# Kernel tuning notes

Measured on AMD Instinct MI355X. Metric: run time of the kernel, lower is better.

## Reference

```python
import jax, jax.numpy as jnp
import numpy as np

HIDDEN = 2048
IN = 2
OUT = 2
T = 1024


def setup_inputs() -> dict:
    key = jax.random.key(0)
    ks = jax.random.split(key, 8)
    s_ih = 1.0 / np.sqrt(HIDDEN)
    return {
        "features": jax.random.normal(ks[0], (1, HIDDEN), dtype=jnp.float32),
        "point_cloud": jax.random.normal(ks[1], (1, T, IN), dtype=jnp.float32),
        "W_ih": jax.random.uniform(ks[2], (4 * HIDDEN, IN), jnp.float32, -s_ih, s_ih),
        "W_hh": jax.random.uniform(ks[3], (4 * HIDDEN, HIDDEN), jnp.float32, -s_ih, s_ih),
        "b_ih": jax.random.uniform(ks[4], (4 * HIDDEN,), jnp.float32, -s_ih, s_ih),
        "b_hh": jax.random.uniform(ks[5], (4 * HIDDEN,), jnp.float32, -s_ih, s_ih),
        "W_fc": jax.random.uniform(ks[6], (OUT, HIDDEN), jnp.float32, -s_ih, s_ih),
        "b_fc": jax.random.uniform(ks[7], (OUT,), jnp.float32, -s_ih, s_ih),
        "max_seq_len": T,
    }


def reference(features, point_cloud, W_ih, W_hh, b_ih, b_hh, W_fc, b_fc, max_seq_len):
    # Training branch of DecoderRNN.forward: teacher-forced LSTMCell decode.
    H = features.shape[1]
    c0 = jnp.zeros_like(features)  # [B, H]

    def step(carry, x_t):
        h, c = carry
        gates = x_t @ W_ih.T + b_ih + h @ W_hh.T + b_hh  # [B, 4H]
        i, f, g, o = jnp.split(gates, 4, axis=-1)  # PyTorch LSTMCell gate order
        c_new = jax.nn.sigmoid(f) * c + jax.nn.sigmoid(i) * jnp.tanh(g)
        h_new = jax.nn.sigmoid(o) * jnp.tanh(c_new)
        out = h_new @ W_fc.T + b_fc  # [B, OUT]
        return (h_new, c_new), out

    xs = jnp.swapaxes(point_cloud, 0, 1)  # [T, B, IN]
    _, outs = jax.lax.scan(step, (features, c0), xs)  # outs: [T, B, OUT]
    # original returns outputs[:, 1:, :] which drops the initial zeros row
    return jnp.swapaxes(outs, 0, 1)  # [B, T, OUT]
```

## Files before the change

### kernel.cpp

```cpp
#include <hip/hip_runtime.h>
#include <math.h>
#include <stdint.h>

#define HIDDEN 2048
#define TSTEPS 1024
#define NWG 256
#define TPB 512
#define UPW 8
#define CPT 16
#define FLAG_STRIDE 32

__device__ __forceinline__ float sigmoidf_(float x) { return 1.0f / (1.0f + __expf(-x)); }

__global__ __launch_bounds__(TPB, 2)
void lstm_hist(const float* __restrict__ features,
               const float* __restrict__ pc,
               const float* __restrict__ W_ih,
               const float* __restrict__ W_hh,
               const float* __restrict__ b_ih,
               const float* __restrict__ b_hh,
               const float* __restrict__ W_fc,
               const float* __restrict__ b_fc,
               float* __restrict__ out,
               int*   __restrict__ flags,
               int*   __restrict__ go,
               float* __restrict__ hhist)
{
    const int b    = blockIdx.x;
    const int t    = threadIdx.x;
    const int lane = t & 63;
    const int wave = t >> 6;

    __builtin_amdgcn_fence(__ATOMIC_ACQUIRE, "agent");

    const int g    = t & 3;
    const int cc   = t >> 2;
    const int col0 = cc * CPT;
    const bool watcher = (b == NWG - 1) && (wave == 0);

    __shared__ float pc_sh[2 * TSTEPS];
    __shared__ float red[8 * 32];
    __shared__ float outred[16];

    {
        const float4* p4 = reinterpret_cast<const float4*>(pc);
        reinterpret_cast<float4*>(pc_sh)[t] = p4[t];
    }

    float w[UPW][CPT];
    {
        const int baserow = g * HIDDEN + b * UPW;
        #pragma unroll
        for (int ji = 0; ji < UPW; ++ji) {
            const float4* src = reinterpret_cast<const float4*>(
                W_hh + (size_t)(baserow + ji) * HIDDEN + col0);
            float4 a0 = src[0], a1 = src[1], a2 = src[2], a3 = src[3];
            w[ji][0]  = a0.x; w[ji][1]  = a0.y; w[ji][2]  = a0.z; w[ji][3]  = a0.w;
            w[ji][4]  = a1.x; w[ji][5]  = a1.y; w[ji][6]  = a1.z; w[ji][7]  = a1.w;
            w[ji][8]  = a2.x; w[ji][9]  = a2.y; w[ji][10] = a2.z; w[ji][11] = a2.w;
            w[ji][12] = a3.x; w[ji][13] = a3.y; w[ji][14] = a3.z; w[ji][15] = a3.w;
        }
    }

    float bias_r = 0.0f, wi0_r = 0.0f, wi1_r = 0.0f, creg = 0.0f;
    if (wave == 0) {
        const int l   = lane & 31;
        const int row = (l >> 3) * HIDDEN + b * UPW + (l & 7);
        bias_r = b_ih[row] + b_hh[row];
        wi0_r  = W_ih[row * 2 + 0];
        wi1_r  = W_ih[row * 2 + 1];
    }
    __syncthreads();

    for (int s = 0; s < TSTEPS; ++s) {
        const int rot = (s >= 1) && (b == ((s - 1) & 255));
        const float* hsrc = (s == 0) ? features : (hhist + (size_t)s * HIDDEN);

        float hr[CPT];
        #pragma unroll
        for (int k = 0; k < CPT; k += 4) {
            float4 hv = *reinterpret_cast<const float4*>(hsrc + col0 + k);
            hr[k] = hv.x; hr[k + 1] = hv.y; hr[k + 2] = hv.z; hr[k + 3] = hv.w;
        }

        float acc[UPW];
        #pragma unroll
        for (int ji = 0; ji < UPW; ++ji) acc[ji] = 0.0f;
        #pragma unroll
        for (int k = 0; k < CPT; ++k) {
            #pragma unroll
            for (int ji = 0; ji < UPW; ++ji) acc[ji] += w[ji][k] * hr[k];
        }
        #pragma unroll
        for (int m = 4; m < 64; m <<= 1) {
            #pragma unroll
            for (int ji = 0; ji < UPW; ++ji) acc[ji] += __shfl_xor(acc[ji], m);
        }
        if (lane < 4) {
            #pragma unroll
            for (int ji = 0; ji < UPW; ++ji) red[wave * 32 + lane * 8 + ji] = acc[ji];
        }

        if (rot) {
            float po0 = 0.0f, po1 = 0.0f;
            #pragma unroll
            for (int k = 0; k < CPT; ++k) {
                po0 += hr[k] * W_fc[col0 + k];
                po1 += hr[k] * W_fc[HIDDEN + col0 + k];
            }
            #pragma unroll
            for (int m = 1; m < 64; m <<= 1) {
                po0 += __shfl_xor(po0, m);
                po1 += __shfl_xor(po1, m);
            }
            if (lane == 0) { outred[wave * 2 + 0] = po0; outred[wave * 2 + 1] = po1; }
        }
        __syncthreads();

        if (wave == 0) {
            const int l = lane & 31;
            float sum = 0.0f;
            #pragma unroll
            for (int ww = 0; ww < 8; ++ww) sum += red[ww * 32 + l];
            const float x0 = pc_sh[2 * s], x1 = pc_sh[2 * s + 1];
            const float gate = sum + bias_r + wi0_r * x0 + wi1_r * x1;
            const float iv = __shfl(gate, (lane & 7));
            const float fv = __shfl(gate, 8 + (lane & 7));
            const float gv = __shfl(gate, 16 + (lane & 7));
            const float ov = __shfl(gate, 24 + (lane & 7));
            const float cnew = sigmoidf_(fv) * creg + sigmoidf_(iv) * tanhf(gv);
            const float hnew = sigmoidf_(ov) * tanhf(cnew);
            creg = cnew;
            const uint32_t hb = __float_as_uint(hnew);

            const uint32_t lo = __shfl(hb, 2 * (lane & 3));
            const uint32_t hi = __shfl(hb, 2 * (lane & 3) + 1);
            if (lane < 4) {
                const uint64_t qv = (uint64_t)lo | ((uint64_t)hi << 32);
                uint64_t* dst = reinterpret_cast<uint64_t*>(
                    hhist + (size_t)(s + 1) * HIDDEN + b * UPW) + lane;
                __hip_atomic_store(dst, qv, __ATOMIC_RELAXED, __HIP_MEMORY_SCOPE_AGENT);
            }
            asm volatile("s_waitcnt vmcnt(0)" ::: "memory");
            if (lane == 0) {
                __hip_atomic_store(flags + (size_t)b * FLAG_STRIDE, s + 1,
                                   __ATOMIC_RELAXED, __HIP_MEMORY_SCOPE_AGENT);
            }
        }

        if (rot && t == 64) {
            float o0 = 0.0f, o1 = 0.0f;
            #pragma unroll
            for (int ww = 0; ww < 8; ++ww) { o0 += outred[ww * 2]; o1 += outred[ww * 2 + 1]; }
            out[(s - 1) * 2 + 0] = 0.25f * o0 + b_fc[0];
            out[(s - 1) * 2 + 1] = 0.25f * o1 + b_fc[1];
        }

        if (watcher) {
            const int l4 = lane * 4;
            const int* f0p = flags + (size_t)(l4 + 0) * FLAG_STRIDE;
            const int* f1p = flags + (size_t)(l4 + 1) * FLAG_STRIDE;
            const int* f2p = flags + (size_t)(l4 + 2) * FLAG_STRIDE;
            const int* f3p = flags + (size_t)(l4 + 3) * FLAG_STRIDE;
            for (;;) {
                const int f0 = __hip_atomic_load(f0p, __ATOMIC_RELAXED, __HIP_MEMORY_SCOPE_AGENT);
                const int f1 = __hip_atomic_load(f1p, __ATOMIC_RELAXED, __HIP_MEMORY_SCOPE_AGENT);
                const int f2 = __hip_atomic_load(f2p, __ATOMIC_RELAXED, __HIP_MEMORY_SCOPE_AGENT);
                const int f3 = __hip_atomic_load(f3p, __ATOMIC_RELAXED, __HIP_MEMORY_SCOPE_AGENT);
                const bool ok = (f0 >= s + 1) & (f1 >= s + 1) & (f2 >= s + 1) & (f3 >= s + 1);
                if (__all(ok)) break;
            }
            __hip_atomic_store(go + (size_t)lane * FLAG_STRIDE, s + 1,
                               __ATOMIC_RELAXED, __HIP_MEMORY_SCOPE_AGENT);
        }

        if (t == 0) {
            const int* gop = go + (size_t)(b >> 2) * FLAG_STRIDE;
            while (__hip_atomic_load(gop, __ATOMIC_RELAXED,
                                     __HIP_MEMORY_SCOPE_AGENT) < s + 1) {
                __builtin_amdgcn_s_sleep(1);
            }
        }
        __syncthreads();
    }

    if (b == ((TSTEPS - 1) & 255)) {
        const float* hsrc = hhist + (size_t)TSTEPS * HIDDEN;
        float po0 = 0.0f, po1 = 0.0f;
        #pragma unroll
        for (int k = 0; k < CPT; ++k) {
            const float hv = hsrc[col0 + k];
            po0 += hv * W_fc[col0 + k];
            po1 += hv * W_fc[HIDDEN + col0 + k];
        }
        #pragma unroll
        for (int m = 1; m < 64; m <<= 1) {
            po0 += __shfl_xor(po0, m);
            po1 += __shfl_xor(po1, m);
        }
        if (lane == 0) { outred[wave * 2 + 0] = po0; outred[wave * 2 + 1] = po1; }
        __syncthreads();
        if (t == 0) {
            float o0 = 0.0f, o1 = 0.0f;
            #pragma unroll
            for (int ww = 0; ww < 8; ++ww) { o0 += outred[ww * 2]; o1 += outred[ww * 2 + 1]; }
            out[(TSTEPS - 1) * 2 + 0] = 0.25f * o0 + b_fc[0];
            out[(TSTEPS - 1) * 2 + 1] = 0.25f * o1 + b_fc[1];
        }
    }
}

extern "C" void kernel_launch(void* const* d_in, const int* in_sizes, int n_in,
                              void* d_out, int out_size, void* d_ws, size_t ws_size,
                              hipStream_t stream) {
    const float* features = (const float*)d_in[0];
    const float* pc       = (const float*)d_in[1];
    const float* W_ih     = (const float*)d_in[2];
    const float* W_hh     = (const float*)d_in[3];
    const float* b_ih     = (const float*)d_in[4];
    const float* b_hh     = (const float*)d_in[5];
    const float* W_fc     = (const float*)d_in[6];
    const float* b_fc     = (const float*)d_in[7];
    float* out = (float*)d_out;

    const size_t flags_bytes = (size_t)NWG * FLAG_STRIDE * sizeof(int);
    const size_t go_bytes    = (size_t)64 * FLAG_STRIDE * sizeof(int);
    const size_t hh_off      = flags_bytes + go_bytes;

    int*   flags = (int*)d_ws;
    int*   go    = (int*)((char*)d_ws + flags_bytes);
    float* hhist = (float*)((char*)d_ws + hh_off);

    hipMemsetAsync(d_ws, 0, hh_off, stream);

    hipLaunchKernelGGL(lstm_hist, dim3(NWG), dim3(TPB), 0, stream,
                       features, pc, W_ih, W_hh, b_ih, b_hh, W_fc, b_fc,
                       out, flags, go, hhist);
}
```

Before: 3.595 ms.

## Pack tagged h values into per-block messages and have watcher republish hidden state

Each workgroup now writes its eight new hidden values as 16-bit halves packed together with a step tag into six 64-bit words, using parity double buffering. A dedicated watcher wave polls these tagged messages, which removes the separate flag store and its preceding waitcnt. The watcher then writes the values into the h-history buffer and releases the go flags. The spin wait also drops s_sleep. Hidden state is still stored as full fp32 bit patterns, split into two halves per value. The watcher now does more loads and stores, which lengthens its critical path and may cost more than the removed flag round trip.

```diff
diff --git a/kernel.cpp b/kernel.cpp
--- a/kernel.cpp
+++ b/kernel.cpp
@@ -8,7 +8,9 @@
 #define TPB 512
 #define UPW 8
 #define CPT 16
-#define FLAG_STRIDE 32
+#define LINE_QW 6
+#define LINE_STRIDE_QW 16
+#define GO_STRIDE 32
 
 __device__ __forceinline__ float sigmoidf_(float x) { return 1.0f / (1.0f + __expf(-x)); }
 
@@ -22,9 +24,9 @@
                const float* __restrict__ W_fc,
                const float* __restrict__ b_fc,
                float* __restrict__ out,
-               int*   __restrict__ flags,
-               int*   __restrict__ go,
-               float* __restrict__ hhist)
+               uint64_t* __restrict__ msg,
+               int*      __restrict__ go,
+               float*    __restrict__ hhist)
 {
     const int b    = blockIdx.x;
     const int t    = threadIdx.x;
@@ -36,7 +38,6 @@
     const int g    = t & 3;
     const int cc   = t >> 2;
     const int col0 = cc * CPT;
-    const bool watcher = (b == NWG - 1) && (wave == 0);
 
     __shared__ float pc_sh[2 * TSTEPS];
     __shared__ float red[8 * 32];
@@ -116,6 +117,8 @@
             if (lane == 0) { outred[wave * 2 + 0] = po0; outred[wave * 2 + 1] = po1; }
         }
         __syncthreads();
+
+        const int par = ((s + 1) & 1) * 8;
 
         if (wave == 0) {
             const int l = lane & 31;
@@ -133,19 +136,67 @@
             creg = cnew;
             const uint32_t hb = __float_as_uint(hnew);
 
-            const uint32_t lo = __shfl(hb, 2 * (lane & 3));
-            const uint32_t hi = __shfl(hb, 2 * (lane & 3) + 1);
-            if (lane < 4) {
-                const uint64_t qv = (uint64_t)lo | ((uint64_t)hi << 32);
-                uint64_t* dst = reinterpret_cast<uint64_t*>(
-                    hhist + (size_t)(s + 1) * HIDDEN + b * UPW) + lane;
-                __hip_atomic_store(dst, qv, __ATOMIC_RELAXED, __HIP_MEMORY_SCOPE_AGENT);
+            uint64_t v = ((uint64_t)(uint32_t)(s + 1)) << 48;
+            #pragma unroll
+            for (int i = 0; i < 3; ++i) {
+                const int m  = 3 * lane + i;
+                const int mc = (m < 16) ? m : 15;
+                const uint32_t bits = __shfl(hb, mc >> 1);
+                const uint32_t half = (mc & 1) ? (bits >> 16) : (bits & 0xFFFFu);
+                if (m < 16) v |= (uint64_t)half << (32 - 16 * i);
+            }
+            if (lane < LINE_QW) {
+                __hip_atomic_store(msg + (size_t)b * LINE_STRIDE_QW + par + lane,
+                                   v, __ATOMIC_RELAXED, __HIP_MEMORY_SCOPE_AGENT);
+            }
+        }
+
+        if (b == NWG - 1 && wave == 7) {
+            const int l4 = lane * 4;
+            const uint32_t tagexp = (uint32_t)(s + 1);
+            uint64_t q[4][LINE_QW];
+            for (;;) {
+                #pragma unroll
+                for (int i = 0; i < 4; ++i) {
+                    const uint64_t* lp = msg + (size_t)(l4 + i) * LINE_STRIDE_QW + par;
+                    #pragma unroll
+                    for (int j = 0; j < LINE_QW; ++j) {
+                        q[i][j] = __hip_atomic_load(lp + j, __ATOMIC_RELAXED,
+                                                    __HIP_MEMORY_SCOPE_AGENT);
+                    }
+                }
+                bool ok = true;
+                #pragma unroll
+                for (int i = 0; i < 4; ++i) {
+                    #pragma unroll
+                    for (int j = 0; j < LINE_QW; ++j) {
+                        ok &= ((uint32_t)(q[i][j] >> 48) == tagexp);
+                    }
+                }
+                if (ok) break;
+            }
+            uint64_t* hq = reinterpret_cast<uint64_t*>(hhist + (size_t)(s + 1) * HIDDEN);
+            #pragma unroll
+            for (int i = 0; i < 4; ++i) {
+                uint32_t H[18];
+                #pragma unroll
+                for (int j = 0; j < LINE_QW; ++j) {
+                    H[3 * j + 0] = (uint32_t)(q[i][j] >> 32) & 0xFFFFu;
+                    H[3 * j + 1] = (uint32_t)(q[i][j] >> 16) & 0xFFFFu;
+                    H[3 * j + 2] = (uint32_t)(q[i][j] >>  0) & 0xFFFFu;
+                }
+                #pragma unroll
+                for (int k = 0; k < 4; ++k) {
+                    const uint32_t f0 = H[4 * k + 0] | (H[4 * k + 1] << 16);
+                    const uint32_t f1 = H[4 * k + 2] | (H[4 * k + 3] << 16);
+                    __hip_atomic_store(hq + (size_t)(l4 + i) * 4 + k,
+                                       (uint64_t)f0 | ((uint64_t)f1 << 32),
+                                       __ATOMIC_RELAXED, __HIP_MEMORY_SCOPE_AGENT);
+                }
             }
             asm volatile("s_waitcnt vmcnt(0)" ::: "memory");
-            if (lane == 0) {
-                __hip_atomic_store(flags + (size_t)b * FLAG_STRIDE, s + 1,
-                                   __ATOMIC_RELAXED, __HIP_MEMORY_SCOPE_AGENT);
-            }
+            __hip_atomic_store(go + (size_t)lane * GO_STRIDE, s + 1,
+                               __ATOMIC_RELAXED, __HIP_MEMORY_SCOPE_AGENT);
         }
 
         if (rot && t == 64) {
@@ -156,30 +207,10 @@
             out[(s - 1) * 2 + 1] = 0.25f * o1 + b_fc[1];
         }
 
-        if (watcher) {
-            const int l4 = lane * 4;
-            const int* f0p = flags + (size_t)(l4 + 0) * FLAG_STRIDE;
-            const int* f1p = flags + (size_t)(l4 + 1) * FLAG_STRIDE;
-            const int* f2p = flags + (size_t)(l4 + 2) * FLAG_STRIDE;
-            const int* f3p = flags + (size_t)(l4 + 3) * FLAG_STRIDE;
-            for (;;) {
-                const int f0 = __hip_atomic_load(f0p, __ATOMIC_RELAXED, __HIP_MEMORY_SCOPE_AGENT);
-                const int f1 = __hip_atomic_load(f1p, __ATOMIC_RELAXED, __HIP_MEMORY_SCOPE_AGENT);
-                const int f2 = __hip_atomic_load(f2p, __ATOMIC_RELAXED, __HIP_MEMORY_SCOPE_AGENT);
-                const int f3 = __hip_atomic_load(f3p, __ATOMIC_RELAXED, __HIP_MEMORY_SCOPE_AGENT);
-                const bool ok = (f0 >= s + 1) & (f1 >= s + 1) & (f2 >= s + 1) & (f3 >= s + 1);
-                if (__all(ok)) break;
-            }
-            __hip_atomic_store(go + (size_t)lane * FLAG_STRIDE, s + 1,
-                               __ATOMIC_RELAXED, __HIP_MEMORY_SCOPE_AGENT);
-        }
-
-        if (t == 0) {
-            const int* gop = go + (size_t)(b >> 2) * FLAG_STRIDE;
+        if (t == 0 && b != NWG - 1) {
+            const int* gop = go + (size_t)(b >> 2) * GO_STRIDE;
             while (__hip_atomic_load(gop, __ATOMIC_RELAXED,
-                                     __HIP_MEMORY_SCOPE_AGENT) < s + 1) {
-                __builtin_amdgcn_s_sleep(1);
-            }
+                                     __HIP_MEMORY_SCOPE_AGENT) < s + 1) {}
         }
         __syncthreads();
     }
@@ -223,17 +254,17 @@
     const float* b_fc     = (const float*)d_in[7];
     float* out = (float*)d_out;
 
-    const size_t flags_bytes = (size_t)NWG * FLAG_STRIDE * sizeof(int);
-    const size_t go_bytes    = (size_t)64 * FLAG_STRIDE * sizeof(int);
-    const size_t hh_off      = flags_bytes + go_bytes;
-
-    int*   flags = (int*)d_ws;
-    int*   go    = (int*)((char*)d_ws + flags_bytes);
-    float* hhist = (float*)((char*)d_ws + hh_off);
+    const size_t msg_bytes = (size_t)NWG * LINE_STRIDE_QW * sizeof(uint64_t);
+    const size_t go_bytes  = (size_t)64 * GO_STRIDE * sizeof(int);
+    const size_t hh_off    = msg_bytes + go_bytes;
+
+    uint64_t* msg   = (uint64_t*)d_ws;
+    int*      go    = (int*)((char*)d_ws + msg_bytes);
+    float*    hhist = (float*)((char*)d_ws + hh_off);
 
     hipMemsetAsync(d_ws, 0, hh_off, stream);
 
     hipLaunchKernelGGL(lstm_hist, dim3(NWG), dim3(TPB), 0, stream,
                        features, pc, W_ih, W_hh, b_ih, b_hh, W_fc, b_fc,
-                       out, flags, go, hhist);
+                       out, msg, go, hhist);
 }
```

Measured after the change: 5.983 ms. +66.4%, slower.

## Replace per-step block barrier with per-thread spin on grid go flags

Applied to the files above, without the earlier changes.

The end-of-step __syncthreads and the single-thread sleep-poll on the go flag are removed. Every thread now spins directly on its group's go flag (or on an LDS flag in the watcher block) just before loading the next hidden state. The watcher moves to wave 7 of the last block and also publishes progress through LDS. This targets the latency of the grid-wide step handoff: the barrier and s_sleep wake-up delay. In exchange, all threads poll global memory, which adds memory traffic, and correctness now depends on the flag ordering rather than an explicit barrier for reuse of the shared reduction buffers.

```diff
diff --git a/kernel.cpp b/kernel.cpp
--- a/kernel.cpp
+++ b/kernel.cpp
@@ -9,38 +9,41 @@
 #define UPW 8
 #define CPT 16
 #define FLAG_STRIDE 32
+#define GO_STRIDE 32
 
 __device__ __forceinline__ float sigmoidf_(float x) { return 1.0f / (1.0f + __expf(-x)); }
 
 __global__ __launch_bounds__(TPB, 2)
-void lstm_hist(const float* __restrict__ features,
-               const float* __restrict__ pc,
-               const float* __restrict__ W_ih,
-               const float* __restrict__ W_hh,
-               const float* __restrict__ b_ih,
-               const float* __restrict__ b_hh,
-               const float* __restrict__ W_fc,
-               const float* __restrict__ b_fc,
-               float* __restrict__ out,
-               int*   __restrict__ flags,
-               int*   __restrict__ go,
-               float* __restrict__ hhist)
+void lstm_v10(const float* __restrict__ features,
+              const float* __restrict__ pc,
+              const float* __restrict__ W_ih,
+              const float* __restrict__ W_hh,
+              const float* __restrict__ b_ih,
+              const float* __restrict__ b_hh,
+              const float* __restrict__ W_fc,
+              const float* __restrict__ b_fc,
+              float* __restrict__ out,
+              int*   __restrict__ flags,
+              int*   __restrict__ go,
+              float* __restrict__ hhist)
 {
     const int b    = blockIdx.x;
     const int t    = threadIdx.x;
     const int lane = t & 63;
     const int wave = t >> 6;
-
-    __builtin_amdgcn_fence(__ATOMIC_ACQUIRE, "agent");
-
     const int g    = t & 3;
     const int cc   = t >> 2;
     const int col0 = cc * CPT;
-    const bool watcher = (b == NWG - 1) && (wave == 0);
+    const bool isw255 = (b == NWG - 1);
+
+    __builtin_amdgcn_fence(__ATOMIC_ACQUIRE, "agent");
 
     __shared__ float pc_sh[2 * TSTEPS];
     __shared__ float red[8 * 32];
     __shared__ float outred[16];
+    __shared__ int   ls_go;
+
+    if (t == 0) ls_go = 0;
 
     {
         const float4* p4 = reinterpret_cast<const float4*>(pc);
@@ -72,15 +75,32 @@
     }
     __syncthreads();
 
+    const int* gop = go + (size_t)(b >> 2) * GO_STRIDE;
+
     for (int s = 0; s < TSTEPS; ++s) {
         const int rot = (s >= 1) && (b == ((s - 1) & 255));
-        const float* hsrc = (s == 0) ? features : (hhist + (size_t)s * HIDDEN);
 
         float hr[CPT];
-        #pragma unroll
-        for (int k = 0; k < CPT; k += 4) {
-            float4 hv = *reinterpret_cast<const float4*>(hsrc + col0 + k);
-            hr[k] = hv.x; hr[k + 1] = hv.y; hr[k + 2] = hv.z; hr[k + 3] = hv.w;
+        if (s == 0) {
+            #pragma unroll
+            for (int k = 0; k < CPT; k += 4) {
+                float4 hv = *reinterpret_cast<const float4*>(features + col0 + k);
+                hr[k] = hv.x; hr[k + 1] = hv.y; hr[k + 2] = hv.z; hr[k + 3] = hv.w;
+            }
+        } else {
+            if (isw255) {
+                while (__hip_atomic_load(&ls_go, __ATOMIC_RELAXED,
+                                         __HIP_MEMORY_SCOPE_WORKGROUP) < s) {}
+            } else {
+                while (__hip_atomic_load(gop, __ATOMIC_RELAXED,
+                                         __HIP_MEMORY_SCOPE_AGENT) < s) {}
+            }
+            const float* hsrc = hhist + (size_t)s * HIDDEN;
+            #pragma unroll
+            for (int k = 0; k < CPT; k += 4) {
+                float4 hv = *reinterpret_cast<const float4*>(hsrc + col0 + k);
+                hr[k] = hv.x; hr[k + 1] = hv.y; hr[k + 2] = hv.z; hr[k + 3] = hv.w;
+            }
         }
 
         float acc[UPW];
@@ -148,15 +168,7 @@
             }
         }
 
-        if (rot && t == 64) {
-            float o0 = 0.0f, o1 = 0.0f;
-            #pragma unroll
-            for (int ww = 0; ww < 8; ++ww) { o0 += outred[ww * 2]; o1 += outred[ww * 2 + 1]; }
-            out[(s - 1) * 2 + 0] = 0.25f * o0 + b_fc[0];
-            out[(s - 1) * 2 + 1] = 0.25f * o1 + b_fc[1];
-        }
-
-        if (watcher) {
+        if (isw255 && wave == 7) {
             const int l4 = lane * 4;
             const int* f0p = flags + (size_t)(l4 + 0) * FLAG_STRIDE;
             const int* f1p = flags + (size_t)(l4 + 1) * FLAG_STRIDE;
@@ -170,21 +182,26 @@
                 const bool ok = (f0 >= s + 1) & (f1 >= s + 1) & (f2 >= s + 1) & (f3 >= s + 1);
                 if (__all(ok)) break;
             }
-            __hip_atomic_store(go + (size_t)lane * FLAG_STRIDE, s + 1,
+            __hip_atomic_store(go + (size_t)lane * GO_STRIDE, s + 1,
                                __ATOMIC_RELAXED, __HIP_MEMORY_SCOPE_AGENT);
-        }
-
-        if (t == 0) {
-            const int* gop = go + (size_t)(b >> 2) * FLAG_STRIDE;
-            while (__hip_atomic_load(gop, __ATOMIC_RELAXED,
-                                     __HIP_MEMORY_SCOPE_AGENT) < s + 1) {
-                __builtin_amdgcn_s_sleep(1);
-            }
-        }
-        __syncthreads();
-    }
-
-    if (b == ((TSTEPS - 1) & 255)) {
+            if (lane == 0) {
+                __hip_atomic_store(&ls_go, s + 1, __ATOMIC_RELAXED,
+                                   __HIP_MEMORY_SCOPE_WORKGROUP);
+            }
+        }
+
+        if (rot && t == 64) {
+            float o0 = 0.0f, o1 = 0.0f;
+            #pragma unroll
+            for (int ww = 0; ww < 8; ++ww) { o0 += outred[ww * 2]; o1 += outred[ww * 2 + 1]; }
+            out[(s - 1) * 2 + 0] = 0.25f * o0 + b_fc[0];
+            out[(s - 1) * 2 + 1] = 0.25f * o1 + b_fc[1];
+        }
+    }
+
+    if (isw255) {
+        while (__hip_atomic_load(&ls_go, __ATOMIC_RELAXED,
+                                 __HIP_MEMORY_SCOPE_WORKGROUP) < TSTEPS) {}
         const float* hsrc = hhist + (size_t)TSTEPS * HIDDEN;
         float po0 = 0.0f, po1 = 0.0f;
         #pragma unroll
@@ -224,7 +241,7 @@
     float* out = (float*)d_out;
 
     const size_t flags_bytes = (size_t)NWG * FLAG_STRIDE * sizeof(int);
-    const size_t go_bytes    = (size_t)64 * FLAG_STRIDE * sizeof(int);
+    const size_t go_bytes    = (size_t)64 * GO_STRIDE * sizeof(int);
     const size_t hh_off      = flags_bytes + go_bytes;
 
     int*   flags = (int*)d_ws;
@@ -233,7 +250,7 @@
 
     hipMemsetAsync(d_ws, 0, hh_off, stream);
 
-    hipLaunchKernelGGL(lstm_hist, dim3(NWG), dim3(TPB), 0, stream,
+    hipLaunchKernelGGL(lstm_v10, dim3(NWG), dim3(TPB), 0, stream,
                        features, pc, W_ih, W_hh, b_ih, b_hh, W_fc, b_fc,
                        out, flags, go, hhist);
 }
```

Measured after the change: 3.614 ms. Within noise of the previous version (+0.5%).
